# Kernel tuning notes

Measured on AMD Instinct MI355X. Metric: run time of the kernel, lower is better.

## Reference

```python
import math
import jax, jax.numpy as jnp
import numpy as np

BS = 4; C = 128; D = 128; NH = 4; NL = 2; NP = 8
SHAPES = [(64, 96), (32, 48)]            # (H, W) per level
STARTS = [0, SHAPES[0][0] * SHAPES[0][1]]  # level_start_index


def lrelu(x):
    return jnp.where(x >= 0, x, 0.1 * x)


def conv2d(x, w, b):
    y = jax.lax.conv_general_dilated(x, w, (1, 1), [(1, 1), (1, 1)],
                                     dimension_numbers=('NCHW', 'OIHW', 'NCHW'))
    return y + b[None, :, None, None]


def pos_enc_sine(bs, H, W, npf=64, T=10000.0):
    # DETR PositionEmbeddingSine (normalize=True), mask of ones -> cumsum = index+1
    scale = 2.0 * math.pi
    eps = 1e-6
    y = (jnp.arange(1, H + 1, dtype=jnp.float32) / (H + eps) * scale)[:, None]
    x = (jnp.arange(1, W + 1, dtype=jnp.float32) / (W + eps) * scale)[None, :]
    y = jnp.broadcast_to(y, (H, W))
    x = jnp.broadcast_to(x, (H, W))
    dim_t = T ** (2.0 * (jnp.arange(npf) // 2).astype(jnp.float32) / npf)
    px = x[..., None] / dim_t
    py = y[..., None] / dim_t
    def interleave(p):
        return jnp.stack([jnp.sin(p[..., 0::2]), jnp.cos(p[..., 1::2])], -1).reshape(H, W, npf)
    pos = jnp.concatenate([interleave(py), interleave(px)], -1)  # [H,W,2*npf]
    return jnp.broadcast_to(pos.transpose(2, 0, 1)[None], (bs, 2 * npf, H, W))


def ref_points(bs, H, W):
    ys = (jnp.arange(H, dtype=jnp.float32) + 0.5) / H
    xs = (jnp.arange(W, dtype=jnp.float32) + 0.5) / W
    gy, gx = jnp.meshgrid(ys, xs, indexing='ij')
    ref = jnp.stack([gx.reshape(-1), gy.reshape(-1)], -1)  # [hw, 2] (x, y)
    return jnp.broadcast_to(ref[None, :, None, :], (bs, H * W, 1, 2))


def sample_level(v, loc, Hl, Wl):
    # v: [bs, Hl*Wl, nh, d]; loc: [bs, nq, nh, np, 2] in [0,1] -> grid_sample bilinear, zero pad
    bs, nq, nh, npts, _ = loc.shape
    d = v.shape[-1]
    x = loc[..., 0] * Wl - 0.5
    y = loc[..., 1] * Hl - 0.5
    x0f = jnp.floor(x); y0f = jnp.floor(y)
    fx = x - x0f; fy = y - y0f
    x0 = x0f.astype(jnp.int32); y0 = y0f.astype(jnp.int32)
    def gather(xi, yi):
        valid = (xi >= 0) & (xi < Wl) & (yi >= 0) & (yi < Hl)
        idx = jnp.clip(yi, 0, Hl - 1) * Wl + jnp.clip(xi, 0, Wl - 1)  # [bs,nq,nh,np]
        idx = idx.transpose(0, 1, 3, 2).reshape(bs, nq * npts, nh)
        g = jnp.take_along_axis(v, idx[..., None], axis=1)  # [bs,nq*np,nh,d]
        g = g.reshape(bs, nq, npts, nh, d).transpose(0, 1, 3, 2, 4)  # [bs,nq,nh,np,d]
        return g * valid[..., None]
    w00 = (1 - fx) * (1 - fy); w01 = fx * (1 - fy); w10 = (1 - fx) * fy; w11 = fx * fy
    return (gather(x0, y0) * w00[..., None] + gather(x0 + 1, y0) * w01[..., None]
            + gather(x0, y0 + 1) * w10[..., None] + gather(x0 + 1, y0 + 1) * w11[..., None])


def msda(value, loc, weights):
    # value [bs,Nv,nh,d], loc [bs,nq,nh,nl,np,2], weights [bs,nq,nh,nl,np]
    out = 0.0
    for l, (Hl, Wl) in enumerate(SHAPES):
        v_l = value[:, STARTS[l]:STARTS[l] + Hl * Wl]
        s = sample_level(v_l, loc[:, :, :, l], Hl, Wl)  # [bs,nq,nh,np,d]
        out = out + jnp.einsum('bqhpd,bqhp->bqhd', s, weights[:, :, :, l])
    bs, nq, nh, d = out.shape
    return out.reshape(bs, nq, nh * d)


def block(query, value, qloc, so_w, so_b, aw_w, aw_b, op_w, op_b):
    bs, nq, _ = query.shape
    off = (query @ so_w + so_b).reshape(bs, nq, NH, NL, NP, 2)
    aw = jax.nn.softmax((query @ aw_w + aw_b).reshape(bs, nq, NH, NL * NP), -1)
    aw = aw.reshape(bs, nq, NH, NL, NP)
    norm = jnp.array([[w, h] for (h, w) in SHAPES], jnp.float32)  # [nl,2] = (W,H)
    loc = qloc[:, :, None, :, None, :] + off / norm[None, None, None, :, None, :]
    return msda(value, loc, aw) @ op_w + op_b  # dropout = identity (eval)


def _forward(feat0_l0, feat0_l1, feat1_l0, feat1_l1,
             cw1, cb1, cw2, cb2, cw3, cb3, vw, vb, lvl_emb,
             so_w0, so_b0, aw_w0, aw_b0, op_w0, op_b0,
             so_w1, so_b1, aw_w1, aw_b1, op_w1, op_b1):
    bs = feat0_l0.shape[0]
    H1, W1 = SHAPES[-1]
    # scale_conv stem on feature0_list[-1]
    q = lrelu(conv2d(feat0_l1, cw1, cb1))
    q = lrelu(conv2d(q, cw2, cb2))
    q = lrelu(conv2d(q, cw3, cb3))
    q = q + pos_enc_sine(bs, H1, W1, npf=D // 2)
    qloc = ref_points(bs, H1, W1)  # [bs, hw, 1, 2]
    # flatten levels + level embeds
    f0 = jnp.concatenate([f.reshape(bs, C, -1) + lvl_emb[l][None, :, None]
                          for l, f in enumerate([feat0_l0, feat0_l1])], axis=2)
    f1 = jnp.concatenate([f.reshape(bs, C, -1) + lvl_emb[l][None, :, None]
                          for l, f in enumerate([feat1_l0, feat1_l1])], axis=2)
    cat = jnp.concatenate([f0, f1], axis=1)  # [bs, 2C, Nv]
    value = jnp.einsum('oc,bcn->bno', vw, cat) + vb  # 1x1 Conv1d -> [bs, Nv, D]
    value = jnp.broadcast_to(value[:, :, None, :], (bs, value.shape[1], NH, D))
    query = q.reshape(bs, D, -1).transpose(0, 2, 1)  # [bs, hw, D]
    query = block(query, value, qloc, so_w0, so_b0, aw_w0, aw_b0, op_w0, op_b0)
    query = block(query, value, qloc, so_w1, so_b1, aw_w1, aw_b1, op_w1, op_b1)
    return query.reshape(bs, H1, W1, D).transpose(0, 3, 1, 2)


def setup_inputs() -> dict:
    key = jax.random.key(0)
    ks = iter(jax.random.split(key, 32))
    def rn(shape, s=1.0):
        return jax.random.normal(next(ks), shape, jnp.float32) * s
    inp = {}
    inp['feat0_l0'] = rn((BS, C, SHAPES[0][0], SHAPES[0][1]))
    inp['feat0_l1'] = rn((BS, C, SHAPES[1][0], SHAPES[1][1]))
    inp['feat1_l0'] = rn((BS, C, SHAPES[0][0], SHAPES[0][1]))
    inp['feat1_l1'] = rn((BS, C, SHAPES[1][0], SHAPES[1][1]))
    inp['cw1'] = rn((2 * D, C, 3, 3), 0.03); inp['cb1'] = rn((2 * D,), 0.01)
    inp['cw2'] = rn((D, 2 * D, 3, 3), 0.03); inp['cb2'] = rn((D,), 0.01)
    inp['cw3'] = rn((D, D, 3, 3), 0.03); inp['cb3'] = rn((D,), 0.01)
    inp['vw'] = rn((D, 2 * C), 0.05); inp['vb'] = rn((D,), 0.01)
    inp['lvl_emb'] = rn((NL, C), 0.05)
    for i in range(2):
        inp[f'so_w{i}'] = rn((D, NH * NL * NP * 2), 0.02)
        inp[f'so_b{i}'] = rn((NH * NL * NP * 2,), 0.5)
        inp[f'aw_w{i}'] = rn((D, NH * NL * NP), 0.02)
        inp[f'aw_b{i}'] = rn((NH * NL * NP,), 0.01)
        inp[f'op_w{i}'] = rn((NH * D, D), 0.05)
        inp[f'op_b{i}'] = rn((D,), 0.01)
    return inp


def reference(feat0_l0, feat0_l1, feat1_l0, feat1_l1,
              cw1, cb1, cw2, cb2, cw3, cb3, vw, vb, lvl_emb,
              so_w0, so_b0, aw_w0, aw_b0, op_w0, op_b0,
              so_w1, so_b1, aw_w1, aw_b1, op_w1, op_b1):
    return _forward(feat0_l0, feat0_l1, feat1_l0, feat1_l1,
                    cw1, cb1, cw2, cb2, cw3, cb3, vw, vb, lvl_emb,
                    so_w0, so_b0, aw_w0, aw_b0, op_w0, op_b0,
                    so_w1, so_b1, aw_w1, aw_b1, op_w1, op_b1)
```

## Files before the change

### kernel.cpp

```cpp
#include <hip/hip_runtime.h>
#include <hip/hip_bf16.h>

typedef unsigned short u16;
typedef u16   u16x8 __attribute__((ext_vector_type(8)));
typedef short s16x8 __attribute__((ext_vector_type(8)));
typedef float f32x4 __attribute__((ext_vector_type(4)));

__device__ __forceinline__ float bf2f(u16 u) {
    union { unsigned int i; float f; } v; v.i = ((unsigned int)u) << 16; return v.f;
}
__device__ __forceinline__ u16 f2bf(float f) {
    unsigned int x = __float_as_uint(f);
    return (u16)((x + 0x7fffu + ((x >> 16) & 1u)) >> 16);
}
__device__ __forceinline__ float ldv(const void* p, size_t i, int f32) {
    return f32 ? ((const float*)p)[i] : bf2f(((const u16*)p)[i]);
}

struct P21 { const void* p[21]; };

struct Args {
    P21 a;
    const void *f00, *f01, *f10, *f11;
    u16 *AW1, *AW2, *AW3, *AVW, *APJ0, *APJ1, *AOP1, *BPJ0, *BPJ1, *SB;
    u16 *OPW0, *ZB, *W1, *B1;
    u16 *CATT, *X0, *VAL, *CH1, *CH2, *QT0, *S;
    float* PA;
};

template<int ACT, int OUTM, int OUT_BF16, int BN>
__device__ __forceinline__ void gemm_body(
    u16* __restrict__ smem, int bid,
    const u16* __restrict__ A, const u16* __restrict__ Bt,
    const u16* __restrict__ bias, void* __restrict__ Cv,
    int M, int K, int ldc, int nbase, int f32o)
{
    constexpr int NF = BN >> 4;
    u16 (*As)[72] = (u16(*)[72])smem;
    u16 (*Bs)[72] = (u16(*)[72])(smem + 4608);

    const int t    = threadIdx.x;
    const int wv   = t >> 6, lane = t & 63;
    const int fr   = lane & 15, fg = lane >> 4;
    const int tiles_m = M >> 6;
    const int bm = bid % tiles_m, bn = bid / tiles_m;
    const int m0 = bm << 6, n0 = bn * BN;

    f32x4 acc[NF] = {};
    const int srow = t >> 2;
    const int scol = (t & 3) << 4;
    const int brow = (BN == 64) ? srow : (t >> 3);
    const int bcol = (BN == 64) ? scol : ((t & 7) << 3);
    const u16* Ap = A  + (size_t)(m0 + srow) * K + scol;
    const u16* Bp = Bt + (size_t)(n0 + brow) * K + bcol;

    const int ns = K >> 6;
    uint4 av0 = *(const uint4*)Ap, av1 = *(const uint4*)(Ap + 8);
    uint4 bv0 = *(const uint4*)Bp, bv1 = {0,0,0,0};
    if constexpr (BN == 64) bv1 = *(const uint4*)(Bp + 8);
    for (int s = 0; s < ns; ++s) {
        __syncthreads();
        *(uint4*)&As[srow][scol]     = av0;  *(uint4*)&As[srow][scol + 8] = av1;
        *(uint4*)&Bs[brow][bcol]     = bv0;
        if constexpr (BN == 64) *(uint4*)&Bs[brow][bcol + 8] = bv1;
        __syncthreads();
        if (s + 1 < ns) {
            const u16* An = Ap + ((s + 1) << 6);
            const u16* Bn = Bp + ((s + 1) << 6);
            av0 = *(const uint4*)An;  av1 = *(const uint4*)(An + 8);
            bv0 = *(const uint4*)Bn;
            if constexpr (BN == 64) bv1 = *(const uint4*)(Bn + 8);
        }
        union U { uint4 q; s16x8 v; };
        #pragma unroll
        for (int kk = 0; kk < 2; ++kk) {
            U af; af.q = *(const uint4*)&As[(wv << 4) + fr][(kk << 5) + (fg << 3)];
            U bf[NF];
            #pragma unroll
            for (int j = 0; j < NF; ++j)
                bf[j].q = *(const uint4*)&Bs[(j << 4) + fr][(kk << 5) + (fg << 3)];
            #pragma unroll
            for (int j = 0; j < NF; ++j)
                acc[j] = __builtin_amdgcn_mfma_f32_16x16x32_bf16(af.v, bf[j].v, acc[j], 0, 0, 0);
        }
    }

    float vv[NF][4];
    #pragma unroll
    for (int r = 0; r < 4; ++r) {
        float bvv = bf2f(bias[m0 + (wv << 4) + (fg << 2) + r]);
        #pragma unroll
        for (int j = 0; j < NF; ++j) {
            float v = acc[j][r] + bvv;
            if (ACT) v = (v >= 0.f) ? v : 0.1f * v;
            vv[j][r] = v;
        }
    }

    if constexpr (OUTM == 0) {
        #pragma unroll
        for (int j = 0; j < NF; ++j)
            #pragma unroll
            for (int r = 0; r < 4; ++r) {
                size_t idx = (size_t)(m0 + (wv << 4) + (fg << 2) + r) * ldc
                           + (nbase + n0 + (j << 4) + fr);
                if (OUT_BF16) ((u16*)Cv)[idx] = f2bf(vv[j][r]);
                else          ((float*)Cv)[idx] = vv[j][r];
            }
    } else if constexpr (OUTM == 1) {
        __syncthreads();
        u16* bb = smem;
        #pragma unroll
        for (int j = 0; j < NF; ++j)
            #pragma unroll
            for (int r = 0; r < 4; ++r)
                bb[((j << 4) + fr) * 72 + (wv << 4) + (fg << 2) + r] = f2bf(vv[j][r]);
        __syncthreads();
        if constexpr (BN == 64) {
            int row = t >> 2, seg = (t & 3) << 4;
            const uint4* src = (const uint4*)&bb[row * 72 + seg];
            uint4* dst = (uint4*)((u16*)Cv + (size_t)(nbase + n0 + row) * M + m0 + seg);
            dst[0] = src[0];
            dst[1] = src[1];
        } else {
            int row = t >> 3, seg = (t & 7) << 3;
            const uint4* src = (const uint4*)&bb[row * 72 + seg];
            uint4* dst = (uint4*)((u16*)Cv + (size_t)(nbase + n0 + row) * M + m0 + seg);
            dst[0] = src[0];
        }
    } else {
        __syncthreads();
        constexpr int LDB = BN + 8;
        u16* bb = smem;
        #pragma unroll
        for (int j = 0; j < NF; ++j)
            #pragma unroll
            for (int r = 0; r < 4; ++r)
                bb[((wv << 4) + (fg << 2) + r) * LDB + (j << 4) + fr] = f2bf(vv[j][r]);
        __syncthreads();
        constexpr int EPT = BN / 4;
        int mrow = t >> 2, seg = (t & 3) * EPT;
        int b = n0 / 1536, hw0 = (n0 % 1536) + seg;
        size_t base = (size_t)(b * 128 + m0 + mrow) * 1536 + hw0;
        if (!f32o) {
            #pragma unroll
            for (int q = 0; q < EPT / 8; ++q)
                *(uint4*)((u16*)Cv + base + q * 8) = *(const uint4*)&bb[mrow * LDB + seg + q * 8];
        } else {
            float* dst = (float*)Cv + base;
            #pragma unroll
            for (int j = 0; j < EPT; ++j) dst[j] = bf2f(bb[mrow * LDB + seg + j]);
        }
    }
}

template<int CIN, int POS, int BN>
__device__ __forceinline__ void conv_body(
    u16* __restrict__ smem, int bid,
    const u16* __restrict__ A, const u16* __restrict__ X,
    const u16* __restrict__ bias, u16* __restrict__ Cv, int M)
{
    constexpr int NF = BN >> 4;
    u16 (*As)[72] = (u16(*)[72])smem;
    u16 (*Bs)[72] = (u16(*)[72])(smem + 4608);

    constexpr int NK2 = CIN / 64;
    constexpr int TOT = 9 * NK2;

    const int t    = threadIdx.x;
    const int wv   = t >> 6, lane = t & 63;
    const int fr   = lane & 15, fg = lane >> 4;
    const int tiles_m = M >> 6;
    const int bm = bid % tiles_m, bn = bid / tiles_m;
    const int m0 = bm << 6, n0 = bn * BN;

    const int srow = t >> 2;
    const int scol = (t & 3) << 4;
    const int brow = (BN == 64) ? srow : (t >> 3);
    const int bcol = (BN == 64) ? scol : ((t & 7) << 3);
    const int n  = n0 + brow;
    const int hw = n % 1536;
    const int hp = hw / 48, wp = hw % 48;
    const u16* Ar = A + (size_t)(m0 + srow) * (9 * CIN) + scol;

    f32x4 acc[NF] = {};

    auto ld = [&](int s, uint4& a0, uint4& a1, uint4& b0, uint4& b1) {
        int tap = s / NK2, k0 = (s % NK2) << 6;
        int dy = tap / 3 - 1, dx = tap % 3 - 1;
        bool vr = ((unsigned)(hp + dy) < 32u) && ((unsigned)(wp + dx) < 48u);
        const u16* Ap = Ar + tap * CIN + k0;
        a0 = *(const uint4*)Ap;  a1 = *(const uint4*)(Ap + 8);
        if (vr) {
            const u16* Bp = X + (size_t)(n + dy * 48 + dx) * CIN + bcol + k0;
            b0 = *(const uint4*)Bp;
            if constexpr (BN == 64) b1 = *(const uint4*)(Bp + 8);
        } else {
            b0 = uint4{0,0,0,0};  b1 = uint4{0,0,0,0};
        }
    };

    uint4 av0, av1, bv0, bv1;
    ld(0, av0, av1, bv0, bv1);
    for (int s = 0; s < TOT; ++s) {
        __syncthreads();
        *(uint4*)&As[srow][scol]     = av0;  *(uint4*)&As[srow][scol + 8] = av1;
        *(uint4*)&Bs[brow][bcol]     = bv0;
        if constexpr (BN == 64) *(uint4*)&Bs[brow][bcol + 8] = bv1;
        __syncthreads();
        if (s + 1 < TOT) ld(s + 1, av0, av1, bv0, bv1);
        union U { uint4 q; s16x8 v; };
        #pragma unroll
        for (int kk = 0; kk < 2; ++kk) {
            U af; af.q = *(const uint4*)&As[(wv << 4) + fr][(kk << 5) + (fg << 3)];
            U bf[NF];
            #pragma unroll
            for (int j = 0; j < NF; ++j)
                bf[j].q = *(const uint4*)&Bs[(j << 4) + fr][(kk << 5) + (fg << 3)];
            #pragma unroll
            for (int j = 0; j < NF; ++j)
                acc[j] = __builtin_amdgcn_mfma_f32_16x16x32_bf16(af.v, bf[j].v, acc[j], 0, 0, 0);
        }
    }

    float vv[NF][4];
    #pragma unroll
    for (int r = 0; r < 4; ++r) {
        float bvv = bf2f(bias[m0 + (wv << 4) + (fg << 2) + r]);
        #pragma unroll
        for (int j = 0; j < NF; ++j) {
            float v = acc[j][r] + bvv;
            vv[j][r] = (v >= 0.f) ? v : 0.1f * v;
        }
    }

    if (POS) {
        const float TWO_PI = 6.283185307179586f;
        #pragma unroll
        for (int j = 0; j < NF; ++j) {
            int ntok = n0 + (j << 4) + fr;
            int hw2 = ntok % 1536;
            int hp2 = hw2 / 48, wp2 = hw2 % 48;
            float yv = (float)(hp2 + 1) * (TWO_PI / (32.f + 1e-6f));
            float xv = (float)(wp2 + 1) * (TWO_PI / (48.f + 1e-6f));
            #pragma unroll
            for (int r = 0; r < 4; ++r) {
                int d = m0 + (wv << 4) + (fg << 2) + r;
                int mm = (d & 63) >> 1;
                float dim = exp2f((float)mm * (13.287712379549449f / 32.f));
                float val = ((d < 64) ? yv : xv) / dim;
                vv[j][r] += (d & 1) ? cosf(val) : sinf(val);
            }
        }
    }

    __syncthreads();
    u16* bb = smem;
    #pragma unroll
    for (int j = 0; j < NF; ++j)
        #pragma unroll
        for (int r = 0; r < 4; ++r)
            bb[((j << 4) + fr) * 72 + (wv << 4) + (fg << 2) + r] = f2bf(vv[j][r]);
    __syncthreads();
    if constexpr (BN == 64) {
        int row = t >> 2, seg = (t & 3) << 4;
        const uint4* src = (const uint4*)&bb[row * 72 + seg];
        uint4* dst = (uint4*)(Cv + (size_t)(n0 + row) * M + m0 + seg);
        dst[0] = src[0];
        dst[1] = src[1];
    } else {
        int row = t >> 3, seg = (t & 7) << 3;
        const uint4* src = (const uint4*)&bb[row * 72 + seg];
        uint4* dst = (uint4*)(Cv + (size_t)(n0 + row) * M + m0 + seg);
        dst[0] = src[0];
    }
}

template<int ACT, int OUTM, int OUT_BF16, int BN>
__global__ __launch_bounds__(256) void gemm_kn(
    const u16* __restrict__ A, const u16* __restrict__ Bt,
    const u16* __restrict__ bias, void* __restrict__ Cv,
    int M, int K, int ldc, int nbase, const int* __restrict__ flag)
{
    __shared__ __align__(16) u16 smem[9216];
    int f32o = (OUTM == 2) ? *flag : 0;
    gemm_body<ACT, OUTM, OUT_BF16, BN>(smem, blockIdx.x, A, Bt, bias, Cv, M, K, ldc, nbase, f32o);
}

template<int CIN, int POS, int BN>
__global__ __launch_bounds__(256) void conv_gemm(
    const u16* __restrict__ A, const u16* __restrict__ X,
    const u16* __restrict__ bias, u16* __restrict__ Cv, int M)
{
    __shared__ __align__(16) u16 smem[9216];
    conv_body<CIN, POS, BN>(smem, blockIdx.x, A, X, bias, Cv, M);
}

__global__ __launch_bounds__(256) void val_conv1_k(Args g)
{
    __shared__ __align__(16) u16 smem[9216];
    int bid = blockIdx.x;
    u16* cb1 = g.SB;
    u16* vb  = g.SB + 512;
    u16* ob0 = g.SB + 896;
    if (bid < 960) {
        gemm_body<0, 1, 1, 64>(smem, bid, g.AVW, g.CATT, vb, g.VAL, 128, 256, 0, 0, 0);
    } else if (bid < 1344) {
        conv_body<128, 0, 64>(smem, bid - 960, g.AW1, g.X0, cb1, g.CH1, 256);
    } else if (bid < 1392) {
        gemm_body<0, 0, 1, 32>(smem, bid - 1344, g.APJ1, g.OPW0, g.ZB, g.W1, 192, 128, 512, 0, 0);
    } else {
        int m = threadIdx.x;
        if (m < 192) {
            float s = bf2f(g.BPJ1[m]);
            const u16* row = g.APJ1 + (size_t)m * 128;
            for (int k = 0; k < 128; ++k) s += bf2f(row[k]) * bf2f(ob0[k]);
            g.B1[m] = f2bf(s);
        }
    }
}

__global__ __launch_bounds__(256) void prep_fused(Args g, int* __restrict__ FLAG)
{
    __shared__ __align__(16) u16 Ts[128 * 66];
    const int t = threadIdx.x;
    const P21& a = g.a;
    unsigned int w = ((const unsigned int*)g.f00)[t];
    float pa = fabsf(bf2f((u16)(w & 0xFFFFu)));
    int cnt = __syncthreads_count(pa > 1e-6f && pa < 1e4f);
    const int f32 = (cnt < 128);
    const int bid = blockIdx.x;
    if (bid == 0 && t == 0) *FLAG = f32;

    if (bid < 3975) {
        int gg = bid * 256 + t;
        if (gg < 294912) { int m = gg / 1152, rem = gg % 1152, tap = rem >> 7, ci = rem & 127;
            g.AW1[gg] = f2bf(ldv(a.p[0], (size_t)m * 1152 + ci * 9 + tap, f32)); return; }
        gg -= 294912;
        if (gg < 294912) { int m = gg / 2304, rem = gg % 2304, tap = rem >> 8, ci = rem & 255;
            g.AW2[gg] = f2bf(ldv(a.p[2], (size_t)m * 2304 + ci * 9 + tap, f32)); return; }
        gg -= 294912;
        if (gg < 147456) { int m = gg / 1152, rem = gg % 1152, tap = rem >> 7, ci = rem & 127;
            g.AW3[gg] = f2bf(ldv(a.p[4], (size_t)m * 1152 + ci * 9 + tap, f32)); return; }
        gg -= 147456;
        if (gg < 32768) { g.AVW[gg] = f2bf(ldv(a.p[6], gg, f32)); return; }
        gg -= 32768;
        if (gg < 24576) { int o = gg >> 7, d = gg & 127;
            g.APJ0[gg] = f2bf(o < 128 ? ldv(a.p[9], d * 128 + o, f32)
                                      : ldv(a.p[11], d * 64 + (o - 128), f32)); return; }
        gg -= 24576;
        if (gg < 24576) { int o = gg >> 7, d = gg & 127;
            g.APJ1[gg] = f2bf(o < 128 ? ldv(a.p[15], d * 128 + o, f32)
                                      : ldv(a.p[17], d * 64 + (o - 128), f32)); return; }
        gg -= 24576;
        if (gg < 65536) { int o = gg >> 9, k = gg & 511; g.AOP1[gg] = f2bf(ldv(a.p[19], k * 128 + o, f32)); return; }
        gg -= 65536;
        if (gg < 192) { g.BPJ0[gg] = f2bf(gg < 128 ? ldv(a.p[10], gg, f32) : ldv(a.p[12], gg - 128, f32)); return; }
        gg -= 192;
        if (gg < 192) { g.BPJ1[gg] = f2bf(gg < 128 ? ldv(a.p[16], gg, f32) : ldv(a.p[18], gg - 128, f32)); return; }
        gg -= 192;
        if (gg < 1152) {
            const int off[8] = {0, 256, 384, 512, 640, 896, 1024, 1152};
            const int src[7] = {1, 3, 5, 7, 8, 14, 20};
            int s = 0;
            #pragma unroll
            for (int i = 1; i < 7; ++i) s += (gg >= off[i]);
            g.SB[gg] = f2bf(ldv(a.p[src[s]], gg - off[s], f32)); return;
        }
        gg -= 1152;
        if (gg < 65536) { g.OPW0[gg] = f2bf(ldv(a.p[13], gg, f32)); return; }
        gg -= 65536;
        if (gg < 192) { g.ZB[gg] = 0; return; }
        return;
    }

    const void* src; u16* dst;
    int b, hw0, HW, rowlen, coloff, lvl, addemb;
    if (bid < 4935) {
        int gg = bid - 3975;
        int half = gg & 1;  gg >>= 1;
        b = gg / 120;  int tile = gg % 120;
        lvl = (tile >= 96) ? 1 : 0;
        int tl = lvl ? tile - 96 : tile;
        hw0 = tl << 6;
        HW = lvl ? 1536 : 6144;
        src = (half == 0) ? (lvl ? g.f01 : g.f00) : (lvl ? g.f11 : g.f10);
        dst = g.CATT + (size_t)(b * 7680 + lvl * 6144 + hw0) * 256;
        rowlen = 256; coloff = half << 7; addemb = 1;
    } else {
        int gg = bid - 4935;
        b = gg / 24;  hw0 = (gg % 24) << 6;
        HW = 1536; src = g.f01;
        dst = g.X0 + (size_t)(b * 1536 + hw0) * 128;
        rowlen = 128; coloff = 0; lvl = 1; addemb = 0;
    }

    {
        int c = t >> 1, hseg = (t & 1) << 5;
        size_t base = (size_t)(b * 128 + c) * HW + hw0 + hseg;
        u16* dstl = &Ts[c * 66 + hseg];
        if (!f32) {
            const u16* s8 = (const u16*)src + base;
            *(uint4*)(dstl)      = *(const uint4*)(s8);
            *(uint4*)(dstl + 8)  = *(const uint4*)(s8 + 8);
            *(uint4*)(dstl + 16) = *(const uint4*)(s8 + 16);
            *(uint4*)(dstl + 24) = *(const uint4*)(s8 + 24);
        } else {
            const float* sf = (const float*)src + base;
            #pragma unroll
            for (int q = 0; q < 32; ++q) dstl[q] = f2bf(sf[q]);
        }
    }
    __syncthreads();
    {
        int tok = t & 63, cseg = (t >> 6) << 5;
        u16 outv[32];
        #pragma unroll
        for (int j = 0; j < 32; ++j) {
            float x = bf2f(Ts[(cseg + j) * 66 + tok]);
            if (addemb) x += ldv(a.p[8], lvl * 128 + cseg + j, f32);
            outv[j] = f2bf(x);
        }
        u16* drow = dst + (size_t)tok * rowlen + coloff + cseg;
        #pragma unroll
        for (int q = 0; q < 4; ++q)
            *(uint4*)(drow + q * 8) = *(const uint4*)(&outv[q * 8]);
    }
}

__global__ void msda_sample(const float* __restrict__ PA, const u16* __restrict__ VAL,
                            u16* __restrict__ S)
{
    __shared__ int   SMI[4][64];
    __shared__ float SMW[4][64];
    __shared__ float LG[64];
    __shared__ float EW[64];
    int bid = blockIdx.x;
    int tok = ((bid & 7) * 768) + (bid >> 3);
    int t = threadIdx.x;
    int b = tok / 1536, hw = tok % 1536;
    int hp = hw / 48, wp = hw % 48;

    if (t < 64) {
        int l = (t >> 3) & 1, p = t & 7, h = t >> 4;
        int orow = h * 32 + l * 16 + p * 2;
        float offx = PA[(size_t)orow * 6144 + tok];
        float offy = PA[(size_t)(orow + 1) * 6144 + tok];
        LG[t]      = PA[(size_t)(128 + h * 16 + l * 8 + p) * 6144 + tok];
        float Wl = l ? 48.f : 96.f, Hl = l ? 32.f : 64.f;
        int iWl = l ? 48 : 96, iHl = l ? 32 : 64;
        int base = l ? 6144 : 0;
        float locx = (wp + 0.5f) / 48.f + offx / Wl;
        float locy = (hp + 0.5f) / 32.f + offy / Hl;
        float x = locx * Wl - 0.5f;
        float y = locy * Hl - 0.5f;
        float xf = floorf(x), yf = floorf(y);
        float fx = x - xf, fy = y - yf;
        int ix = (int)xf, iy = (int)yf;
        int vrow = b * 7680 + base;
        float w00 = (1.f - fx) * (1.f - fy), w01 = fx * (1.f - fy);
        float w10 = (1.f - fx) * fy,         w11 = fx * fy;
        bool vx0 = (unsigned)ix < (unsigned)iWl,       vx1 = (unsigned)(ix + 1) < (unsigned)iWl;
        bool vy0 = (unsigned)iy < (unsigned)iHl,       vy1 = (unsigned)(iy + 1) < (unsigned)iHl;
        SMI[0][t] = (vx0 && vy0) ? vrow + iy * iWl + ix           : 0;
        SMI[1][t] = (vx1 && vy0) ? vrow + iy * iWl + ix + 1       : 0;
        SMI[2][t] = (vx0 && vy1) ? vrow + (iy + 1) * iWl + ix     : 0;
        SMI[3][t] = (vx1 && vy1) ? vrow + (iy + 1) * iWl + ix + 1 : 0;
        SMW[0][t] = (vx0 && vy0) ? w00 : 0.f;
        SMW[1][t] = (vx1 && vy0) ? w01 : 0.f;
        SMW[2][t] = (vx0 && vy1) ? w10 : 0.f;
        SMW[3][t] = (vx1 && vy1) ? w11 : 0.f;
    }
    __syncthreads();
    if (t < 64) {
        int h0 = t & ~15;
        float mx = -1e30f;
        for (int i = 0; i < 16; ++i) mx = fmaxf(mx, LG[h0 + i]);
        EW[t] = expf(LG[t] - mx);
    }
    __syncthreads();
    if (t < 64) {
        int h0 = t & ~15;
        float sum = 0.f;
        for (int i = 0; i < 16; ++i) sum += EW[h0 + i];
        float aw = EW[t] / sum;
        SMW[0][t] *= aw; SMW[1][t] *= aw;
        SMW[2][t] *= aw; SMW[3][t] *= aw;
    }
    __syncthreads();

    const int h = t >> 5, sub = t & 31, dseg = sub & 15, half = sub >> 4;
    const u16* Vb = VAL + (size_t)dseg * 8;
    float acc[8] = {0.f, 0.f, 0.f, 0.f, 0.f, 0.f, 0.f, 0.f};
    #pragma unroll
    for (int rr = 0; rr < 32; rr += 16) {
        u16x8 vreg[16];
        float wreg[16];
        #pragma unroll
        for (int q = 0; q < 16; ++q) {
            int pr = (half << 5) + rr + q;
            int s = pr >> 2, c = pr & 3;
            wreg[q] = SMW[c][(h << 4) + s];
            vreg[q] = *(const u16x8*)(Vb + (size_t)SMI[c][(h << 4) + s] * 128);
        }
        #pragma unroll
        for (int q = 0; q < 16; ++q)
            #pragma unroll
            for (int j = 0; j < 8; ++j) acc[j] += wreg[q] * bf2f(vreg[q][j]);
    }
    #pragma unroll
    for (int j = 0; j < 8; ++j) acc[j] += __shfl_xor(acc[j], 16, 64);
    if (!half) {
        u16x8 o;
        #pragma unroll
        for (int j = 0; j < 8; ++j) o[j] = f2bf(acc[j]);
        *(u16x8*)(S + (size_t)tok * 512 + (h << 7) + (dseg << 3)) = o;
    }
}

extern "C" void kernel_launch(void* const* d_in, const int* in_sizes, int n_in,
                              void* d_out, int out_size, void* d_ws, size_t ws_size,
                              hipStream_t stream)
{
    (void)in_sizes; (void)n_in; (void)out_size; (void)ws_size;

    char* ws = (char*)d_ws;
    size_t off = 0;
    auto alloc = [&](size_t bytes) { size_t o = off; off += (bytes + 255) & ~(size_t)255; return o; };
    int*   FLAG = (int*)(ws + alloc(256));
    u16*   AW1  = (u16*)(ws + alloc(294912ull * 2));
    u16*   AW2  = (u16*)(ws + alloc(294912ull * 2));
    u16*   AW3  = (u16*)(ws + alloc(147456ull * 2));
    u16*   AVW  = (u16*)(ws + alloc(32768ull * 2));
    u16*   APJ0 = (u16*)(ws + alloc(24576ull * 2));
    u16*   APJ1 = (u16*)(ws + alloc(24576ull * 2));
    u16*   AOP1 = (u16*)(ws + alloc(65536ull * 2));
    u16*   BPJ0 = (u16*)(ws + alloc(512));
    u16*   BPJ1 = (u16*)(ws + alloc(512));
    u16*   SB   = (u16*)(ws + alloc(1152ull * 2));
    u16*   OPW0 = (u16*)(ws + alloc(65536ull * 2));
    u16*   ZB   = (u16*)(ws + alloc(512));
    u16*   W1   = (u16*)(ws + alloc(98304ull * 2));
    u16*   B1   = (u16*)(ws + alloc(512));
    u16*   VAL  = (u16*)(ws + alloc(30720ull * 128 * 2));
    u16*   X0   = (u16*)(ws + alloc(6144ull * 128 * 2));
    u16*   CH1  = (u16*)(ws + alloc(6144ull * 256 * 2));
    u16*   CH2  = (u16*)(ws + alloc(6144ull * 128 * 2));
    u16*   QT0  = (u16*)(ws + alloc(6144ull * 128 * 2));
    char*  R    = ws + alloc(30720ull * 256 * 2);
    u16*   CATT = (u16*)R;
    float* PA   = (float*)R;
    u16*   S    = (u16*)(R + 192ull * 6144 * 4);

    u16* cb2C = SB + 256;  u16* cb3C = SB + 384;
    u16* ob1C = SB + 1024;

    Args g;
    const int widx[21] = {4,5,6,7,8,9,10,11,12, 13,14,15,16,17,18, 19,20,21,22,23,24};
    for (int i = 0; i < 21; ++i) g.a.p[i] = d_in[widx[i]];
    g.f00 = d_in[0]; g.f01 = d_in[1]; g.f10 = d_in[2]; g.f11 = d_in[3];
    g.AW1 = AW1; g.AW2 = AW2; g.AW3 = AW3; g.AVW = AVW;
    g.APJ0 = APJ0; g.APJ1 = APJ1; g.AOP1 = AOP1;
    g.BPJ0 = BPJ0; g.BPJ1 = BPJ1; g.SB = SB;
    g.OPW0 = OPW0; g.ZB = ZB; g.W1 = W1; g.B1 = B1;
    g.CATT = CATT; g.X0 = X0; g.VAL = VAL; g.CH1 = CH1; g.CH2 = CH2;
    g.QT0 = QT0; g.S = S; g.PA = PA;

    prep_fused<<<5031, 256, 0, stream>>>(g, FLAG);

    val_conv1_k<<<1393, 256, 0, stream>>>(g);

    conv_gemm<256, 0, 32><<<2 * 192, 256, 0, stream>>>(AW2, CH1, cb2C, CH2, 128);
    conv_gemm<128, 1, 32><<<2 * 192, 256, 0, stream>>>(AW3, CH2, cb3C, QT0, 128);

    gemm_kn<0, 0, 0, 32><<<3 * 192, 256, 0, stream>>>(APJ0, QT0, BPJ0, PA, 192, 128, 6144, 0, FLAG);
    msda_sample<<<6144, 128, 0, stream>>>(PA, VAL, S);

    gemm_kn<0, 0, 0, 32><<<3 * 192, 256, 0, stream>>>(W1, S, B1, PA, 192, 512, 6144, 0, FLAG);
    msda_sample<<<6144, 128, 0, stream>>>(PA, VAL, S);

    gemm_kn<0, 2, 1, 32><<<2 * 192, 256, 0, stream>>>(AOP1, S, ob1C, d_out, 128, 512, 0, 0, FLAG);
}
```

Baseline: 142.1 us.

## Fuse third conv with positional encoding and sampling-offset projection

Replaces the third 3x3 conv kernel and the following projection GEMM with one kernel. Each block computes all 128 output channels for 16 tokens, adds bias, leaky ReLU and the sine positional encoding, stages the query tile in shared memory, then multiplies it by the 192x128 projection weights and writes the fp32 offsets and weights directly. This removes one launch and the round trip of the QT0 intermediate through global memory. In exchange each block covers only 16 tokens, so B-tile reuse is lower, and the projection weights are read straight from global memory by every block.

```diff
diff --git a/kernel.cpp b/kernel.cpp
--- a/kernel.cpp
+++ b/kernel.cpp
@@ -24,7 +24,7 @@
     const void *f00, *f01, *f10, *f11;
     u16 *AW1, *AW2, *AW3, *AVW, *APJ0, *APJ1, *AOP1, *BPJ0, *BPJ1, *SB;
     u16 *OPW0, *ZB, *W1, *B1;
-    u16 *CATT, *X0, *VAL, *CH1, *CH2, *QT0, *S;
+    u16 *CATT, *X0, *VAL, *CH1, *CH2, *S;
     float* PA;
 };
 
@@ -154,7 +154,7 @@
     }
 }
 
-template<int CIN, int POS, int BN>
+template<int CIN, int BN>
 __device__ __forceinline__ void conv_body(
     u16* __restrict__ smem, int bid,
     const u16* __restrict__ A, const u16* __restrict__ X,
@@ -231,26 +231,6 @@
         for (int j = 0; j < NF; ++j) {
             float v = acc[j][r] + bvv;
             vv[j][r] = (v >= 0.f) ? v : 0.1f * v;
-        }
-    }
-
-    if (POS) {
-        const float TWO_PI = 6.283185307179586f;
-        #pragma unroll
-        for (int j = 0; j < NF; ++j) {
-            int ntok = n0 + (j << 4) + fr;
-            int hw2 = ntok % 1536;
-            int hp2 = hw2 / 48, wp2 = hw2 % 48;
-            float yv = (float)(hp2 + 1) * (TWO_PI / (32.f + 1e-6f));
-            float xv = (float)(wp2 + 1) * (TWO_PI / (48.f + 1e-6f));
-            #pragma unroll
-            for (int r = 0; r < 4; ++r) {
-                int d = m0 + (wv << 4) + (fg << 2) + r;
-                int mm = (d & 63) >> 1;
-                float dim = exp2f((float)mm * (13.287712379549449f / 32.f));
-                float val = ((d < 64) ? yv : xv) / dim;
-                vv[j][r] += (d & 1) ? cosf(val) : sinf(val);
-            }
         }
     }
 
@@ -287,13 +267,117 @@
     gemm_body<ACT, OUTM, OUT_BF16, BN>(smem, blockIdx.x, A, Bt, bias, Cv, M, K, ldc, nbase, f32o);
 }
 
-template<int CIN, int POS, int BN>
+template<int CIN, int BN>
 __global__ __launch_bounds__(256) void conv_gemm(
     const u16* __restrict__ A, const u16* __restrict__ X,
     const u16* __restrict__ bias, u16* __restrict__ Cv, int M)
 {
     __shared__ __align__(16) u16 smem[9216];
-    conv_body<CIN, POS, BN>(smem, blockIdx.x, A, X, bias, Cv, M);
+    conv_body<CIN, BN>(smem, blockIdx.x, A, X, bias, Cv, M);
+}
+
+__global__ __launch_bounds__(256) void conv3_proj(
+    const u16* __restrict__ AW3, const u16* __restrict__ X,
+    const u16* __restrict__ cb3, const u16* __restrict__ APJ0,
+    const u16* __restrict__ BPJ0, float* __restrict__ PA)
+{
+    __shared__ __align__(16) u16 As[128 * 72];
+    __shared__ __align__(16) u16 Bs[16 * 72];
+    __shared__ __align__(16) u16 qs[16 * 136];
+
+    const int t  = threadIdx.x;
+    const int wv = t >> 6, lane = t & 63;
+    const int fr = lane & 15, fg = lane >> 4;
+    const int n0 = blockIdx.x << 4;
+
+    const int srow = t >> 1, scol = (t & 1) << 5;
+    const int brow = t >> 3, bcol = (t & 7) << 3;
+    const int nb  = n0 + (brow & 15);
+    const int hwb = nb % 1536;
+    const int hpb = hwb / 48, wpb = hwb % 48;
+
+    union U { uint4 q; s16x8 v; };
+    f32x4 acc[2] = {};
+
+    auto lda = [&](int s, uint4* av) {
+        int tap = s >> 1, k0 = (s & 1) << 6;
+        const u16* Ap = AW3 + (size_t)srow * 1152 + tap * 128 + k0 + scol;
+        av[0] = *(const uint4*)Ap;        av[1] = *(const uint4*)(Ap + 8);
+        av[2] = *(const uint4*)(Ap + 16); av[3] = *(const uint4*)(Ap + 24);
+    };
+    auto ldb = [&](int s, uint4& bv) {
+        int tap = s >> 1, k0 = (s & 1) << 6;
+        int dy = tap / 3 - 1, dx = tap % 3 - 1;
+        bool vr = (t < 128) && ((unsigned)(hpb + dy) < 32u) && ((unsigned)(wpb + dx) < 48u);
+        if (vr) bv = *(const uint4*)(X + (size_t)(nb + dy * 48 + dx) * 128 + k0 + bcol);
+        else    bv = uint4{0, 0, 0, 0};
+    };
+
+    uint4 av[4]; uint4 bv;
+    lda(0, av); ldb(0, bv);
+    for (int s = 0; s < 18; ++s) {
+        __syncthreads();
+        *(uint4*)&As[srow * 72 + scol]      = av[0];
+        *(uint4*)&As[srow * 72 + scol + 8]  = av[1];
+        *(uint4*)&As[srow * 72 + scol + 16] = av[2];
+        *(uint4*)&As[srow * 72 + scol + 24] = av[3];
+        if (t < 128) *(uint4*)&Bs[brow * 72 + bcol] = bv;
+        __syncthreads();
+        if (s + 1 < 18) { lda(s + 1, av); ldb(s + 1, bv); }
+        #pragma unroll
+        for (int kk = 0; kk < 2; ++kk) {
+            U bf; bf.q = *(const uint4*)&Bs[fr * 72 + (kk << 5) + (fg << 3)];
+            #pragma unroll
+            for (int mj = 0; mj < 2; ++mj) {
+                U af; af.q = *(const uint4*)&As[(((wv << 1) + mj) * 16 + fr) * 72 + (kk << 5) + (fg << 3)];
+                acc[mj] = __builtin_amdgcn_mfma_f32_16x16x32_bf16(af.v, bf.v, acc[mj], 0, 0, 0);
+            }
+        }
+    }
+
+    {
+        const float TWO_PI = 6.283185307179586f;
+        int token = n0 + fr;
+        int hw2 = token % 1536;
+        int hp2 = hw2 / 48, wp2 = hw2 % 48;
+        float yv = (float)(hp2 + 1) * (TWO_PI / (32.f + 1e-6f));
+        float xv = (float)(wp2 + 1) * (TWO_PI / (48.f + 1e-6f));
+        #pragma unroll
+        for (int mj = 0; mj < 2; ++mj)
+            #pragma unroll
+            for (int r = 0; r < 4; ++r) {
+                int m = ((wv << 1) + mj) * 16 + (fg << 2) + r;
+                float v = acc[mj][r] + bf2f(cb3[m]);
+                v = (v >= 0.f) ? v : 0.1f * v;
+                int mm = (m & 63) >> 1;
+                float dim = exp2f((float)mm * (13.287712379549449f / 32.f));
+                float val = ((m < 64) ? yv : xv) / dim;
+                v += (m & 1) ? cosf(val) : sinf(val);
+                qs[fr * 136 + m] = f2bf(v);
+            }
+    }
+    __syncthreads();
+
+    {
+        f32x4 pacc[3] = {};
+        #pragma unroll
+        for (int ks = 0; ks < 4; ++ks) {
+            U bf; bf.q = *(const uint4*)&qs[fr * 136 + ks * 32 + (fg << 3)];
+            #pragma unroll
+            for (int j = 0; j < 3; ++j) {
+                int mrow = ((wv * 3 + j) << 4) + fr;
+                U af; af.q = *(const uint4*)&APJ0[(size_t)mrow * 128 + ks * 32 + (fg << 3)];
+                pacc[j] = __builtin_amdgcn_mfma_f32_16x16x32_bf16(af.v, bf.v, pacc[j], 0, 0, 0);
+            }
+        }
+        #pragma unroll
+        for (int j = 0; j < 3; ++j)
+            #pragma unroll
+            for (int r = 0; r < 4; ++r) {
+                int m = ((wv * 3 + j) << 4) + (fg << 2) + r;
+                PA[(size_t)m * 6144 + n0 + fr] = pacc[j][r] + bf2f(BPJ0[m]);
+            }
+    }
 }
 
 __global__ __launch_bounds__(256) void val_conv1_k(Args g)
@@ -306,7 +390,7 @@
     if (bid < 960) {
         gemm_body<0, 1, 1, 64>(smem, bid, g.AVW, g.CATT, vb, g.VAL, 128, 256, 0, 0, 0);
     } else if (bid < 1344) {
-        conv_body<128, 0, 64>(smem, bid - 960, g.AW1, g.X0, cb1, g.CH1, 256);
+        conv_body<128, 64>(smem, bid - 960, g.AW1, g.X0, cb1, g.CH1, 256);
     } else if (bid < 1392) {
         gemm_body<0, 0, 1, 32>(smem, bid - 1344, g.APJ1, g.OPW0, g.ZB, g.W1, 192, 128, 512, 0, 0);
     } else {
@@ -546,7 +630,6 @@
     u16*   X0   = (u16*)(ws + alloc(6144ull * 128 * 2));
     u16*   CH1  = (u16*)(ws + alloc(6144ull * 256 * 2));
     u16*   CH2  = (u16*)(ws + alloc(6144ull * 128 * 2));
-    u16*   QT0  = (u16*)(ws + alloc(6144ull * 128 * 2));
     char*  R    = ws + alloc(30720ull * 256 * 2);
     u16*   CATT = (u16*)R;
     float* PA   = (float*)R;
@@ -564,18 +647,16 @@
     g.BPJ0 = BPJ0; g.BPJ1 = BPJ1; g.SB = SB;
     g.OPW0 = OPW0; g.ZB = ZB; g.W1 = W1; g.B1 = B1;
     g.CATT = CATT; g.X0 = X0; g.VAL = VAL; g.CH1 = CH1; g.CH2 = CH2;
-    g.QT0 = QT0; g.S = S; g.PA = PA;
+    g.S = S; g.PA = PA;
 
     prep_fused<<<5031, 256, 0, stream>>>(g, FLAG);
 
     val_conv1_k<<<1393, 256, 0, stream>>>(g);
 
-    conv_gemm<256, 0, 32><<<2 * 192, 256, 0, stream>>>(AW2, CH1, cb2C, CH2, 128);
-    conv_gemm<128, 1, 32><<<2 * 192, 256, 0, stream>>>(AW3, CH2, cb3C, QT0, 128);
-
-    gemm_kn<0, 0, 0, 32><<<3 * 192, 256, 0, stream>>>(APJ0, QT0, BPJ0, PA, 192, 128, 6144, 0, FLAG);
+    conv_gemm<256, 32><<<2 * 192, 256, 0, stream>>>(AW2, CH1, cb2C, CH2, 128);
+    conv3_proj<<<384, 256, 0, stream>>>(AW3, CH2, cb3C, APJ0, BPJ0, PA);
+
     msda_sample<<<6144, 128, 0, stream>>>(PA, VAL, S);
-
     gemm_kn<0, 0, 0, 32><<<3 * 192, 256, 0, stream>>>(W1, S, B1, PA, 192, 512, 6144, 0, FLAG);
     msda_sample<<<6144, 128, 0, stream>>>(PA, VAL, S);
 
```

Result: slower. 172.8 us (+21.6%).
